# Kernel optimization log

Hardware: AMD Instinct MI355X
Metric: run time of the kernel (lower is better)

The kernel has to match this reference:

```python
import jax, jax.numpy as jnp
import numpy as np
import math

D_MODEL = 512
N_HEADS = 2
B, S = 2, 1024
THRESHOLD = 0.5  # kwargs default 'sparsity_threshold'


def setup_inputs() -> dict:
    key = jax.random.key(0)
    ks = jax.random.split(key, 10)
    D, H = D_MODEL, D_MODEL // 4
    std = 0.02
    return {
        "x": jax.random.normal(ks[0], (B, S, D), jnp.float32),
        "Wq": jax.random.normal(ks[1], (D, D), jnp.float32) * std,
        "Wk": jax.random.normal(ks[2], (D, D), jnp.float32) * std,
        "Wv": jax.random.normal(ks[3], (D, D), jnp.float32) * std,
        "Wo": jax.random.normal(ks[4], (D, D), jnp.float32) * std,
        "bo": jnp.zeros((D,), jnp.float32),
        "W1": jax.random.normal(ks[5], (D, H), jnp.float32) * std,
        "b1": jnp.zeros((H,), jnp.float32),
        "W2": jax.random.normal(ks[6], (H, 1), jnp.float32) * std,
        "b2": jnp.zeros((1,), jnp.float32),
    }


def reference(x, Wq, Wk, Wv, Wo, bo, W1, b1, W2, b2):
    Bsz, Seq, D = x.shape
    Hn = N_HEADS
    dh = D // Hn

    def split_heads(t):
        return t.reshape(Bsz, Seq, Hn, dh).transpose(0, 2, 1, 3)  # [B,H,S,dh]

    q = split_heads(x @ Wq)
    k = split_heads(x @ Wk)
    v = split_heads(x @ Wv)

    scores = jnp.einsum("bhid,bhjd->bhij", q, k) / math.sqrt(dh)  # [B,H,S,S]

    # head-mean features for the pairwise sparsity predictor (n_heads==2 => 2*dh == D)
    q_mean = q.mean(axis=1)  # [B,S,dh]
    k_mean = k.mean(axis=1)  # [B,S,dh]
    # Linear1 of cat([q_mean_i, k_mean_j]) splits into two halves of W1
    a = q_mean @ W1[:dh]   # [B,S,Dh4]
    c = k_mean @ W1[dh:]   # [B,S,Dh4]
    hidden = jax.nn.relu(a[:, :, None, :] + c[:, None, :, :] + b1)  # [B,S,S,Dh4]
    connection_probs = jax.nn.sigmoid(jnp.squeeze(hidden @ W2, -1) + b2[0])  # [B,S,S]

    mask = connection_probs > THRESHOLD  # [B,S,S]
    scores = jnp.where(mask[:, None, :, :], scores, jnp.float32(-1e9))
    attn = jax.nn.softmax(scores, axis=-1)  # dropout inactive in eval

    out = jnp.einsum("bhij,bhjd->bhid", attn, v)  # [B,H,S,dh]
    out = out.transpose(0, 2, 1, 3).reshape(Bsz, Seq, D)
    out = out @ Wo + bo
    return out
```

## Files before the change

### kernel.cpp

```cpp
#include <hip/hip_runtime.h>


typedef unsigned short u16t;
typedef __bf16 bf16x8 __attribute__((ext_vector_type(8)));
typedef float f32x4 __attribute__((ext_vector_type(4)));

#define B_SZ 2
#define S_SZ 1024
#define D_SZ 512
#define DH 256
#define HH 128

static __device__ __forceinline__ u16t f2b(float f) {
    unsigned int u = __builtin_bit_cast(unsigned int, f);
    u += 0x7FFFu + ((u >> 16) & 1u);
    return (u16t)(u >> 16);
}

static __device__ __forceinline__ f32x4 mfma16(bf16x8 a, bf16x8 b, f32x4 c) {
    return __builtin_amdgcn_mfma_f32_16x16x32_bf16(a, b, c, 0, 0, 0);
}

static __device__ __forceinline__ void gload16(const void* g, void* l) {
    __builtin_amdgcn_global_load_lds(
        (const __attribute__((address_space(1))) void*)g,
        (__attribute__((address_space(3))) void*)l, 16, 0, 0);
}

__global__ __launch_bounds__(256) void k_prep(
    const float* __restrict__ x,
    const float* __restrict__ Wq, const float* __restrict__ Wk,
    const float* __restrict__ Wv, const float* __restrict__ Wo,
    const float* __restrict__ W1,
    u16t* __restrict__ xb, u16t* __restrict__ WT, float* __restrict__ Beff)
{
    __shared__ float smf[1088];
    int bidx = blockIdx.x;
    int t = threadIdx.x;
    if (bidx < 1024) {
        int idx = (bidx * 256 + t) * 4;
        float4 v = *(const float4*)(x + idx);
        u16t* o = xb + idx;
        o[0] = f2b(v.x); o[1] = f2b(v.y); o[2] = f2b(v.z); o[3] = f2b(v.w);
    } else if (bidx < 2048) {
        int t2 = bidx - 1024;
        int z = t2 >> 8, rem = t2 & 255;
        int n0 = (rem & 15) * 32, k0 = (rem >> 4) * 32;
        const float* W = z == 0 ? Wq : z == 1 ? Wk : z == 2 ? Wv : Wo;
        u16t* WTz = WT + (size_t)z * D_SZ * D_SZ;
        float (*tile)[33] = (float(*)[33])smf;
        int r = t >> 3, c4 = (t & 7) * 4;
        float4 v = *(const float4*)(W + (size_t)(k0 + r) * D_SZ + n0 + c4);
        tile[r][c4] = v.x; tile[r][c4 + 1] = v.y; tile[r][c4 + 2] = v.z; tile[r][c4 + 3] = v.w;
        __syncthreads();
        u16t o[4];
        o[0] = f2b(tile[c4][r]); o[1] = f2b(tile[c4 + 1][r]);
        o[2] = f2b(tile[c4 + 2][r]); o[3] = f2b(tile[c4 + 3][r]);
        *(ushort4*)(WTz + (size_t)(n0 + r) * D_SZ + k0 + c4) = *(ushort4*)o;
    } else {
        int k = bidx - 2048;
        float* wm0 = smf;
        float* wm1 = smf + 256;
        const float* wrq = Wq + (size_t)k * D_SZ;
        const float* wrk = Wk + (size_t)k * D_SZ;
        wm0[t & 255] = 0.5f * (wrq[t & 255] + wrq[(t & 255) + DH]);
        wm1[t & 255] = 0.5f * (wrk[t & 255] + wrk[(t & 255) + DH]);
        __syncthreads();
        int half = t >> 7, hcol = t & 127;
        const float* wm = half ? wm1 : wm0;
        const float* W1h = W1 + (half ? (size_t)DH * HH : 0);
        float s = 0.f;
        for (int d = 0; d < 256; ++d) s += wm[d] * W1h[(size_t)d * HH + hcol];
        Beff[(size_t)k * 256 + half * 128 + hcol] = s;
    }
}

template<int MF, int NF>
static __device__ __forceinline__ void gemm_db(
    const u16t* __restrict__ A, int lda, const u16t* __restrict__ B, int ldb,
    int K, int tid, u16t* Als, u16t* Bls, f32x4 acc[MF][NF])
{
    const int w = tid >> 6, lane = tid & 63;
    const int lr = lane & 15, kg = lane >> 4;
    const int srow = lane >> 3, scol = (lane & 7) * 8;
    const int ABUF = MF * 4096;
    const int BBUF = NF * 1024;
    auto stage = [&](int bb, int k0) {
#pragma unroll
        for (int q = 0; q < MF * 2; ++q) {
            int ci = w * (MF * 2) + q;
            gload16(A + (size_t)(ci * 8 + srow) * lda + k0 + scol,
                    Als + bb * ABUF + ci * 512);
        }
#pragma unroll
        for (int q = 0; q < NF / 2; ++q) {
            int cj = w * (NF / 2) + q;
            gload16(B + (size_t)(cj * 8 + srow) * ldb + k0 + scol,
                    Bls + bb * BBUF + cj * 512);
        }
    };
    stage(0, 0);
    __syncthreads();
    const int nt = K / 64;
    for (int t = 0; t < nt; ++t) {
        int cur = t & 1;
        if (t + 1 < nt) stage(cur ^ 1, (t + 1) * 64);
        const u16t* Ab = Als + cur * ABUF;
        const u16t* Bb = Bls + cur * BBUF;
#pragma unroll
        for (int kk = 0; kk < 2; ++kk) {
            bf16x8 af[MF], bfr[NF];
#pragma unroll
            for (int fi = 0; fi < MF; ++fi)
                af[fi] = *(const bf16x8*)(&Ab[(w * (MF * 16) + fi * 16 + lr) * 64 + kk * 32 + kg * 8]);
#pragma unroll
            for (int fj = 0; fj < NF; ++fj)
                bfr[fj] = *(const bf16x8*)(&Bb[(fj * 16 + lr) * 64 + kk * 32 + kg * 8]);
#pragma unroll
            for (int fi = 0; fi < MF; ++fi)
#pragma unroll
                for (int fj = 0; fj < NF; ++fj)
                    acc[fi][fj] = mfma16(af[fi], bfr[fj], acc[fi][fj]);
        }
        __syncthreads();
    }
}


__global__ __launch_bounds__(256) void k_qkvac(
    const u16t* __restrict__ xb, const u16t* __restrict__ WT,
    const float* __restrict__ x, const float* __restrict__ Beff,
    const float* __restrict__ b1,
    u16t* __restrict__ qb, u16t* __restrict__ kb, u16t* __restrict__ vT,
    float* __restrict__ a, float* __restrict__ cc)
{
    __shared__ __align__(16) char sm[49152];
    int bid = blockIdx.x;
    int t = threadIdx.x;
    if (bid < 384) {
        u16t* Als = (u16t*)sm;
        u16t* Bls = (u16t*)(sm + 32768);
        int z = bid / 128, rem = bid & 127;
        int m0 = (rem >> 3) * 128, n0 = (rem & 7) * 64;
        const u16t* A = xb + (size_t)m0 * D_SZ;
        const u16t* Bt = WT + (size_t)z * D_SZ * D_SZ + (size_t)n0 * D_SZ;
        f32x4 acc[2][4] = {};
        gemm_db<2, 4>(A, D_SZ, Bt, D_SZ, D_SZ, t, Als, Bls, acc);
        int w = t >> 6, lane = t & 63, lr = lane & 15, kg = lane >> 4;
        if (z < 2) {
            u16t (*vls)[68] = (u16t(*)[68])sm;
            float scale = z == 0 ? 0.0625f : 1.0f;
#pragma unroll
            for (int fi = 0; fi < 2; ++fi)
#pragma unroll
                for (int fj = 0; fj < 4; ++fj)
#pragma unroll
                    for (int rr = 0; rr < 4; ++rr)
                        vls[w * 32 + fi * 16 + kg * 4 + rr][fj * 16 + lr]
                            = f2b(acc[fi][fj][rr] * scale);
            __syncthreads();
            u16t* dst = z == 0 ? qb : kb;
            int c8 = (t & 7) * 8, r0 = t >> 3;
#pragma unroll
            for (int p = 0; p < 4; ++p) {
                int r = r0 + p * 32;
                *(uint4*)(dst + (size_t)(m0 + r) * D_SZ + n0 + c8) = *(const uint4*)(&vls[r][c8]);
            }
        } else {
            u16t (*vls)[136] = (u16t(*)[136])sm;
#pragma unroll
            for (int fi = 0; fi < 2; ++fi)
#pragma unroll
                for (int fj = 0; fj < 4; ++fj)
#pragma unroll
                    for (int rr = 0; rr < 4; ++rr)
                        vls[fj * 16 + lr][w * 32 + fi * 16 + kg * 4 + rr] = f2b(acc[fi][fj][rr]);
            __syncthreads();
            int b = m0 >> 10, s0 = m0 & 1023;
            int cr = t >> 2, seg = t & 3;
            const u16t* srcp = &vls[cr][seg * 32];
            u16t* dstp = vT + (((size_t)(b * D_SZ + n0 + cr)) << 10) + s0 + seg * 32;
#pragma unroll
            for (int qq = 0; qq < 4; ++qq)
                *(uint4*)(dstp + qq * 8) = *(const uint4*)(srcp + qq * 8);
        }
    } else {
        float (*xs)[68] = (float(*)[68])sm;
        float (*bsT)[68] = (float(*)[68])(sm + 17408);
        int t2 = bid - 384;
        int r0 = (t2 & 31) * 64, n0 = (t2 >> 5) * 32;
        int ti = t >> 4, tj = t & 15;
        float acc[4][2] = {};
        for (int k0 = 0; k0 < 512; k0 += 64) {
            if (k0) __syncthreads();
#pragma unroll
            for (int p = 0; p < 4; ++p) {
                int idx = t + p * 256;
                int r = idx >> 4, c4 = (idx & 15) * 4;
                *(float4*)&xs[r][c4] = *(const float4*)(x + (size_t)(r0 + r) * D_SZ + k0 + c4);
            }
#pragma unroll
            for (int p = 0; p < 2; ++p) {
                int idx = t + p * 256;
                int k = idx >> 3, n4 = (idx & 7) * 4;
                float4 v = *(const float4*)(Beff + (size_t)(k0 + k) * 256 + n0 + n4);
                bsT[n4][k] = v.x; bsT[n4 + 1][k] = v.y; bsT[n4 + 2][k] = v.z; bsT[n4 + 3][k] = v.w;
            }
            __syncthreads();
#pragma unroll
            for (int kk = 0; kk < 16; ++kk) {
                float4 xv[4], bv[2];
#pragma unroll
                for (int ri = 0; ri < 4; ++ri) xv[ri] = *(const float4*)&xs[ti + 16 * ri][kk * 4];
#pragma unroll
                for (int rj = 0; rj < 2; ++rj) bv[rj] = *(const float4*)&bsT[tj + 16 * rj][kk * 4];
#pragma unroll
                for (int ri = 0; ri < 4; ++ri)
#pragma unroll
                    for (int rj = 0; rj < 2; ++rj)
                        acc[ri][rj] += xv[ri].x * bv[rj].x + xv[ri].y * bv[rj].y
                                     + xv[ri].z * bv[rj].z + xv[ri].w * bv[rj].w;
            }
        }
        bool isA = n0 < 128;
#pragma unroll
        for (int rj = 0; rj < 2; ++rj) {
            int col = n0 + tj + 16 * rj;
            float badd = isA ? b1[col] : 0.f;
#pragma unroll
            for (int ri = 0; ri < 4; ++ri) {
                int row = r0 + ti + 16 * ri;
                if (isA) a[(size_t)row * HH + col] = acc[ri][rj] + badd;
                else     cc[(size_t)row * HH + (col - 128)] = acc[ri][rj];
            }
        }
    }
}

__global__ __launch_bounds__(256) void k_mask(
    const float* __restrict__ a, const float* __restrict__ c,
    const float* __restrict__ W2, const float* __restrict__ b2,
    unsigned char* __restrict__ maskb)
{
    __shared__ __align__(16) float at[64][132];
    __shared__ __align__(16) float ct[64][132];
    __shared__ __align__(16) float w2s[128];
    int b = blockIdx.z, i0 = blockIdx.y * 64, j0 = blockIdx.x * 64;
    int t = threadIdx.x;
    if (t < 128) w2s[t] = W2[t];
#pragma unroll
    for (int p = 0; p < 8; ++p) {
        int idx = t + p * 256;
        int r = idx >> 5, c4 = (idx & 31) * 4;
        *(float4*)&at[r][c4] = *(const float4*)(a + ((size_t)(b * S_SZ + i0 + r)) * HH + c4);
        *(float4*)&ct[r][c4] = *(const float4*)(c + ((size_t)(b * S_SZ + j0 + r)) * HH + c4);
    }
    __syncthreads();
    float fb2 = b2[0];
    int ti = t >> 4, tj = t & 15;
    float acc[4][4];
#pragma unroll
    for (int ri = 0; ri < 4; ++ri)
#pragma unroll
        for (int rj = 0; rj < 4; ++rj) acc[ri][rj] = fb2;
#pragma unroll 2
    for (int h4 = 0; h4 < 32; ++h4) {
        float4 av[4], cv[4];
        float4 wv = ((const float4*)w2s)[h4];
#pragma unroll
        for (int ri = 0; ri < 4; ++ri) av[ri] = *(const float4*)&at[ti + 16 * ri][h4 * 4];
#pragma unroll
        for (int rj = 0; rj < 4; ++rj) cv[rj] = *(const float4*)&ct[tj + 16 * rj][h4 * 4];
#pragma unroll
        for (int ri = 0; ri < 4; ++ri)
#pragma unroll
            for (int rj = 0; rj < 4; ++rj) {
                acc[ri][rj] += fmaxf(av[ri].x + cv[rj].x, 0.f) * wv.x;
                acc[ri][rj] += fmaxf(av[ri].y + cv[rj].y, 0.f) * wv.y;
                acc[ri][rj] += fmaxf(av[ri].z + cv[rj].z, 0.f) * wv.z;
                acc[ri][rj] += fmaxf(av[ri].w + cv[rj].w, 0.f) * wv.w;
            }
    }
#pragma unroll
    for (int ri = 0; ri < 4; ++ri)
#pragma unroll
        for (int rj = 0; rj < 4; ++rj) {
            int i = i0 + ti + 16 * ri, j = j0 + tj + 16 * rj;
            maskb[((size_t)b << 20) + ((size_t)i << 10) + j] = acc[ri][rj] > 0.f ? 1 : 0;
        }
}

__global__ __launch_bounds__(256) void k_scores(
    const u16t* __restrict__ qb, const u16t* __restrict__ kb,
    const unsigned char* __restrict__ maskb, u16t* __restrict__ P,
    float* __restrict__ lpart)
{
    __shared__ __align__(16) u16t sm[16384];
    u16t* Als = sm;
    u16t* Bls = sm + 8192;
    int bh = blockIdx.z, b = bh >> 1, h = bh & 1;
    int jb = blockIdx.x;
    int m0 = blockIdx.y * 64, n0 = jb * 64;
    const u16t* A = qb + (size_t)b * S_SZ * D_SZ + (size_t)m0 * D_SZ + h * DH;
    const u16t* Bt = kb + (size_t)b * S_SZ * D_SZ + (size_t)n0 * D_SZ + h * DH;
    f32x4 acc[1][4] = {};
    gemm_db<1, 4>(A, D_SZ, Bt, D_SZ, DH, threadIdx.x, Als, Bls, acc);
    int w = threadIdx.x >> 6, lane = threadIdx.x & 63, lr = lane & 15, kg = lane >> 4;
#pragma unroll
    for (int rr = 0; rr < 4; ++rr) {
        int i = m0 + w * 16 + kg * 4 + rr;
        float rs = 0.f;
#pragma unroll
        for (int fj = 0; fj < 4; ++fj) {
            int j = n0 + fj * 16 + lr;
            bool msk = maskb[((size_t)b << 20) + ((size_t)i << 10) + j] != 0;
            float e = msk ? __expf(acc[0][fj][rr]) : 0.f;
            acc[0][fj][rr] = e;
            rs += e;
        }
        rs += __shfl_xor(rs, 1); rs += __shfl_xor(rs, 2);
        rs += __shfl_xor(rs, 4); rs += __shfl_xor(rs, 8);
        if (lr == 0) lpart[((size_t)(jb * 4 + bh) << 10) + i] = rs;
    }
    __syncthreads();
    u16t (*vls)[68] = (u16t(*)[68])sm;
#pragma unroll
    for (int fj = 0; fj < 4; ++fj)
#pragma unroll
        for (int rr = 0; rr < 4; ++rr)
            vls[w * 16 + kg * 4 + rr][fj * 16 + lr] = f2b(acc[0][fj][rr]);
    __syncthreads();
    int r = threadIdx.x >> 2, c16 = (threadIdx.x & 3) * 16;
    u16t* dstp = P + ((size_t)bh << 20) + ((size_t)(m0 + r) << 10) + n0 + c16;
    *(uint4*)dstp = *(const uint4*)(&vls[r][c16]);
    *(uint4*)(dstp + 8) = *(const uint4*)(&vls[r][c16 + 8]);
}

__global__ __launch_bounds__(256) void k_pv(
    const u16t* __restrict__ P, const u16t* __restrict__ vT,
    const float* __restrict__ lpart, u16t* __restrict__ ao)
{
    __shared__ __align__(16) u16t sm[12288];
    __shared__ float invl[64];
    u16t* Als = sm;
    u16t* Bls = sm + 8192;
    int bh = blockIdx.z, b = bh >> 1, h = bh & 1;
    int m0 = blockIdx.y * 64, n0 = blockIdx.x * 32;
    int t = threadIdx.x;
    if (t < 64) {
        float l = 0.f;
        for (int jb = 0; jb < 16; ++jb)
            l += lpart[((size_t)(jb * 4 + bh) << 10) + m0 + t];
        invl[t] = l > 0.f ? 1.0f / l : 0.f;
    }
    const u16t* A = P + ((size_t)bh << 20) + (size_t)m0 * S_SZ;
    const u16t* Bt = vT + ((size_t)(b * D_SZ + h * DH + n0)) * S_SZ;
    f32x4 acc[1][2] = {};
    gemm_db<1, 2>(A, S_SZ, Bt, S_SZ, S_SZ, t, Als, Bls, acc);
    int w = t >> 6, lane = t & 63, lr = lane & 15, kg = lane >> 4;
    u16t (*ols)[40] = (u16t(*)[40])sm;
#pragma unroll
    for (int fj = 0; fj < 2; ++fj)
#pragma unroll
        for (int rr = 0; rr < 4; ++rr) {
            int rl = w * 16 + kg * 4 + rr;
            ols[rl][fj * 16 + lr] = f2b(acc[0][fj][rr] * invl[rl]);
        }
    __syncthreads();
    int r = t >> 2, c8 = (t & 3) * 8;
    *(uint4*)(ao + ((size_t)(b * S_SZ + m0 + r)) * D_SZ + h * DH + n0 + c8)
        = *(const uint4*)(&ols[r][c8]);
}

__global__ __launch_bounds__(256) void k_out(
    const u16t* __restrict__ ao, const u16t* __restrict__ WoT,
    const float* __restrict__ bo, float* __restrict__ out)
{
    __shared__ __align__(16) u16t sm[12288];
    u16t* Als = sm;
    u16t* Bls = sm + 8192;
    int m0 = blockIdx.y * 64, n0 = blockIdx.x * 32;
    const u16t* A = ao + (size_t)m0 * D_SZ;
    const u16t* Bt = WoT + (size_t)n0 * D_SZ;
    f32x4 acc[1][2] = {};
    gemm_db<1, 2>(A, D_SZ, Bt, D_SZ, D_SZ, threadIdx.x, Als, Bls, acc);
    int w = threadIdx.x >> 6, lane = threadIdx.x & 63, lr = lane & 15, kg = lane >> 4;
    float (*ols)[36] = (float(*)[36])sm;
#pragma unroll
    for (int fj = 0; fj < 2; ++fj)
#pragma unroll
        for (int rr = 0; rr < 4; ++rr) {
            int rl = w * 16 + kg * 4 + rr;
            ols[rl][fj * 16 + lr] = acc[0][fj][rr] + bo[n0 + fj * 16 + lr];
        }
    __syncthreads();
    int r0 = threadIdx.x >> 3, c4 = (threadIdx.x & 7) * 4;
#pragma unroll
    for (int p = 0; p < 2; ++p) {
        int r = r0 + p * 32;
        *(float4*)(out + (size_t)(m0 + r) * D_SZ + n0 + c4) = *(const float4*)(&ols[r][c4]);
    }
}

extern "C" void kernel_launch(void* const* d_in, const int* in_sizes, int n_in,
                              void* d_out, int out_size, void* d_ws, size_t ws_size,
                              hipStream_t stream)
{
    const float* x  = (const float*)d_in[0];
    const float* Wq = (const float*)d_in[1];
    const float* Wk = (const float*)d_in[2];
    const float* Wv = (const float*)d_in[3];
    const float* Wo = (const float*)d_in[4];
    const float* bo = (const float*)d_in[5];
    const float* W1 = (const float*)d_in[6];
    const float* b1 = (const float*)d_in[7];
    const float* W2 = (const float*)d_in[8];
    const float* b2 = (const float*)d_in[9];
    float* out = (float*)d_out;

    char* ws = (char*)d_ws;
    size_t off = 0;
    auto carve = [&](size_t bytes) { void* p = ws + off; off += (bytes + 255) & ~(size_t)255; return p; };
    u16t* xb   = (u16t*)carve((size_t)2048 * 512 * 2);
    u16t* WT   = (u16t*)carve((size_t)4 * 512 * 512 * 2);
    u16t* qb   = (u16t*)carve((size_t)2048 * 512 * 2);
    u16t* kb   = (u16t*)carve((size_t)2048 * 512 * 2);
    u16t* vT   = (u16t*)carve((size_t)2 * 512 * 1024 * 2);
    float* Beff = (float*)carve((size_t)512 * 256 * 4);
    float* a   = (float*)carve((size_t)2048 * 128 * 4);
    float* c   = (float*)carve((size_t)2048 * 128 * 4);
    unsigned char* maskb = (unsigned char*)carve((size_t)2 * 1024 * 1024);
    u16t* P    = (u16t*)carve((size_t)4 * 1024 * 1024 * 2);
    float* lpart = (float*)carve((size_t)16 * 4 * 1024 * 4);
    u16t* ao   = (u16t*)carve((size_t)2048 * 512 * 2);
    (void)ws_size;

    k_prep<<<dim3(2560), dim3(256), 0, stream>>>(x, Wq, Wk, Wv, Wo, W1, xb, WT, Beff);
    k_qkvac<<<dim3(640), dim3(256), 0, stream>>>(xb, WT, x, Beff, b1, qb, kb, vT, a, c);
    k_mask<<<dim3(16, 16, 2), dim3(256), 0, stream>>>(a, c, W2, b2, maskb);
    k_scores<<<dim3(16, 16, 4), dim3(256), 0, stream>>>(qb, kb, maskb, P, lpart);
    k_pv<<<dim3(8, 16, 4), dim3(256), 0, stream>>>(P, vT, lpart, ao);
    k_out<<<dim3(16, 32), dim3(256), 0, stream>>>(ao, WT + (size_t)3 * 512 * 512, bo, out);
}
```

Baseline: 104.8 us.

## Fuse mask predictor into scores kernel and compute both heads per block

The separate mask kernel is merged into the scores kernel. Each block first computes its 64x64 mask tile in shared memory, then runs the QK^T GEMM for both heads over the full 512-wide row, writing exp-scores and partial row sums for each head. This removes one launch and the global mask byte array write/read, and the mask is computed once for both heads. The cost is fewer blocks (512 instead of 1024), larger shared memory use (about 54KB), and more sequential work per block, which may lower occupancy.

After: 103.2 us. No clear change (-1.6%).

```diff
diff --git a/kernel.cpp b/kernel.cpp
--- a/kernel.cpp
+++ b/kernel.cpp
@@ -237,103 +237,143 @@
     }
 }
 
-__global__ __launch_bounds__(256) void k_mask(
+__global__ __launch_bounds__(256) void k_scores(
+    const u16t* __restrict__ qb, const u16t* __restrict__ kb,
     const float* __restrict__ a, const float* __restrict__ c,
     const float* __restrict__ W2, const float* __restrict__ b2,
-    unsigned char* __restrict__ maskb)
-{
-    __shared__ __align__(16) float at[64][132];
-    __shared__ __align__(16) float ct[64][132];
-    __shared__ __align__(16) float w2s[128];
-    int b = blockIdx.z, i0 = blockIdx.y * 64, j0 = blockIdx.x * 64;
+    u16t* __restrict__ P, float* __restrict__ lpart)
+{
+    __shared__ __align__(16) char sm[55296];
+    float (*at)[132] = (float(*)[132])sm;
+    float (*ct)[132] = (float(*)[132])(sm + 33792);
+    unsigned char (*msk)[64] = (unsigned char(*)[64])(sm + 50688);
+    float* w2s = (float*)(sm + 54784);
+    int b = blockIdx.z, mt = blockIdx.y, jb = blockIdx.x;
+    int m0 = mt * 64, j0 = jb * 64;
     int t = threadIdx.x;
     if (t < 128) w2s[t] = W2[t];
 #pragma unroll
     for (int p = 0; p < 8; ++p) {
         int idx = t + p * 256;
         int r = idx >> 5, c4 = (idx & 31) * 4;
-        *(float4*)&at[r][c4] = *(const float4*)(a + ((size_t)(b * S_SZ + i0 + r)) * HH + c4);
-        *(float4*)&ct[r][c4] = *(const float4*)(c + ((size_t)(b * S_SZ + j0 + r)) * HH + c4);
-    }
-    __syncthreads();
+        *(float4*)&at[r][c4] = *(const float4*)(a + ((size_t)(b * S_SZ + m0 + r)) * HH + c4);
+    }
     float fb2 = b2[0];
     int ti = t >> 4, tj = t & 15;
-    float acc[4][4];
-#pragma unroll
-    for (int ri = 0; ri < 4; ++ri)
-#pragma unroll
-        for (int rj = 0; rj < 4; ++rj) acc[ri][rj] = fb2;
+#pragma unroll
+    for (int jh = 0; jh < 2; ++jh) {
+        __syncthreads();
+#pragma unroll
+        for (int p = 0; p < 4; ++p) {
+            int idx = t + p * 256;
+            int r = idx >> 5, c4 = (idx & 31) * 4;
+            *(float4*)&ct[r][c4] =
+                *(const float4*)(c + ((size_t)(b * S_SZ + j0 + jh * 32 + r)) * HH + c4);
+        }
+        __syncthreads();
+        float accm[4][2];
+#pragma unroll
+        for (int ri = 0; ri < 4; ++ri)
+#pragma unroll
+            for (int rj = 0; rj < 2; ++rj) accm[ri][rj] = fb2;
 #pragma unroll 2
-    for (int h4 = 0; h4 < 32; ++h4) {
-        float4 av[4], cv[4];
-        float4 wv = ((const float4*)w2s)[h4];
-#pragma unroll
-        for (int ri = 0; ri < 4; ++ri) av[ri] = *(const float4*)&at[ti + 16 * ri][h4 * 4];
-#pragma unroll
-        for (int rj = 0; rj < 4; ++rj) cv[rj] = *(const float4*)&ct[tj + 16 * rj][h4 * 4];
+        for (int h4 = 0; h4 < 32; ++h4) {
+            float4 wv = ((const float4*)w2s)[h4];
+            float4 av[4], cv[2];
+#pragma unroll
+            for (int ri = 0; ri < 4; ++ri) av[ri] = *(const float4*)&at[ti + 16 * ri][h4 * 4];
+#pragma unroll
+            for (int rj = 0; rj < 2; ++rj) cv[rj] = *(const float4*)&ct[tj + 16 * rj][h4 * 4];
+#pragma unroll
+            for (int ri = 0; ri < 4; ++ri)
+#pragma unroll
+                for (int rj = 0; rj < 2; ++rj) {
+                    accm[ri][rj] += fmaxf(av[ri].x + cv[rj].x, 0.f) * wv.x;
+                    accm[ri][rj] += fmaxf(av[ri].y + cv[rj].y, 0.f) * wv.y;
+                    accm[ri][rj] += fmaxf(av[ri].z + cv[rj].z, 0.f) * wv.z;
+                    accm[ri][rj] += fmaxf(av[ri].w + cv[rj].w, 0.f) * wv.w;
+                }
+        }
 #pragma unroll
         for (int ri = 0; ri < 4; ++ri)
 #pragma unroll
-            for (int rj = 0; rj < 4; ++rj) {
-                acc[ri][rj] += fmaxf(av[ri].x + cv[rj].x, 0.f) * wv.x;
-                acc[ri][rj] += fmaxf(av[ri].y + cv[rj].y, 0.f) * wv.y;
-                acc[ri][rj] += fmaxf(av[ri].z + cv[rj].z, 0.f) * wv.z;
-                acc[ri][rj] += fmaxf(av[ri].w + cv[rj].w, 0.f) * wv.w;
-            }
-    }
-#pragma unroll
-    for (int ri = 0; ri < 4; ++ri)
-#pragma unroll
-        for (int rj = 0; rj < 4; ++rj) {
-            int i = i0 + ti + 16 * ri, j = j0 + tj + 16 * rj;
-            maskb[((size_t)b << 20) + ((size_t)i << 10) + j] = acc[ri][rj] > 0.f ? 1 : 0;
-        }
-}
-
-__global__ __launch_bounds__(256) void k_scores(
-    const u16t* __restrict__ qb, const u16t* __restrict__ kb,
-    const unsigned char* __restrict__ maskb, u16t* __restrict__ P,
-    float* __restrict__ lpart)
-{
-    __shared__ __align__(16) u16t sm[16384];
-    u16t* Als = sm;
-    u16t* Bls = sm + 8192;
-    int bh = blockIdx.z, b = bh >> 1, h = bh & 1;
-    int jb = blockIdx.x;
-    int m0 = blockIdx.y * 64, n0 = jb * 64;
-    const u16t* A = qb + (size_t)b * S_SZ * D_SZ + (size_t)m0 * D_SZ + h * DH;
-    const u16t* Bt = kb + (size_t)b * S_SZ * D_SZ + (size_t)n0 * D_SZ + h * DH;
-    f32x4 acc[1][4] = {};
-    gemm_db<1, 4>(A, D_SZ, Bt, D_SZ, DH, threadIdx.x, Als, Bls, acc);
-    int w = threadIdx.x >> 6, lane = threadIdx.x & 63, lr = lane & 15, kg = lane >> 4;
-#pragma unroll
-    for (int rr = 0; rr < 4; ++rr) {
-        int i = m0 + w * 16 + kg * 4 + rr;
-        float rs = 0.f;
-#pragma unroll
-        for (int fj = 0; fj < 4; ++fj) {
-            int j = n0 + fj * 16 + lr;
-            bool msk = maskb[((size_t)b << 20) + ((size_t)i << 10) + j] != 0;
-            float e = msk ? __expf(acc[0][fj][rr]) : 0.f;
-            acc[0][fj][rr] = e;
-            rs += e;
-        }
-        rs += __shfl_xor(rs, 1); rs += __shfl_xor(rs, 2);
-        rs += __shfl_xor(rs, 4); rs += __shfl_xor(rs, 8);
-        if (lr == 0) lpart[((size_t)(jb * 4 + bh) << 10) + i] = rs;
+            for (int rj = 0; rj < 2; ++rj)
+                msk[ti + 16 * ri][jh * 32 + tj + 16 * rj] = accm[ri][rj] > 0.f ? 1 : 0;
     }
     __syncthreads();
+    u16t* Als = (u16t*)sm;
+    u16t* Bls = (u16t*)(sm + 16384);
+    const u16t* A = qb + (size_t)(b * S_SZ + m0) * D_SZ;
+    const u16t* B = kb + (size_t)(b * S_SZ + j0) * D_SZ;
+    const int w = t >> 6, lane = t & 63, lr = lane & 15, kg = lane >> 4;
+    const int srow = lane >> 3, scol = (lane & 7) * 8;
+    auto stage = [&](int bb, int k0) {
+#pragma unroll
+        for (int q = 0; q < 2; ++q) {
+            int ci = w * 2 + q;
+            gload16(A + (size_t)(ci * 8 + srow) * D_SZ + k0 + scol, Als + bb * 4096 + ci * 512);
+            gload16(B + (size_t)(ci * 8 + srow) * D_SZ + k0 + scol, Bls + bb * 4096 + ci * 512);
+        }
+    };
+    f32x4 acc0[4] = {}, acc1[4] = {};
+    stage(0, 0);
+    __syncthreads();
+#pragma unroll
+    for (int t8 = 0; t8 < 8; ++t8) {
+        int cur = t8 & 1;
+        if (t8 < 7) stage(cur ^ 1, (t8 + 1) * 64);
+        const u16t* Ab = Als + cur * 4096;
+        const u16t* Bb = Bls + cur * 4096;
+#pragma unroll
+        for (int kk = 0; kk < 2; ++kk) {
+            bf16x8 af = *(const bf16x8*)(&Ab[(w * 16 + lr) * 64 + kk * 32 + kg * 8]);
+            bf16x8 bfr[4];
+#pragma unroll
+            for (int fj = 0; fj < 4; ++fj)
+                bfr[fj] = *(const bf16x8*)(&Bb[(fj * 16 + lr) * 64 + kk * 32 + kg * 8]);
+            if (t8 < 4) {
+#pragma unroll
+                for (int fj = 0; fj < 4; ++fj) acc0[fj] = mfma16(af, bfr[fj], acc0[fj]);
+            } else {
+#pragma unroll
+                for (int fj = 0; fj < 4; ++fj) acc1[fj] = mfma16(af, bfr[fj], acc1[fj]);
+            }
+        }
+        __syncthreads();
+    }
     u16t (*vls)[68] = (u16t(*)[68])sm;
 #pragma unroll
-    for (int fj = 0; fj < 4; ++fj)
-#pragma unroll
-        for (int rr = 0; rr < 4; ++rr)
-            vls[w * 16 + kg * 4 + rr][fj * 16 + lr] = f2b(acc[0][fj][rr]);
-    __syncthreads();
-    int r = threadIdx.x >> 2, c16 = (threadIdx.x & 3) * 16;
-    u16t* dstp = P + ((size_t)bh << 20) + ((size_t)(m0 + r) << 10) + n0 + c16;
-    *(uint4*)dstp = *(const uint4*)(&vls[r][c16]);
-    *(uint4*)(dstp + 8) = *(const uint4*)(&vls[r][c16 + 8]);
+    for (int h = 0; h < 2; ++h) {
+#pragma unroll
+        for (int rr = 0; rr < 4; ++rr) {
+            int il = w * 16 + kg * 4 + rr;
+            float rs = 0.f;
+#pragma unroll
+            for (int fj = 0; fj < 4; ++fj) {
+                int jl = fj * 16 + lr;
+                float s = h ? acc1[fj][rr] : acc0[fj][rr];
+                float e = msk[il][jl] ? __expf(s) : 0.f;
+                if (h) acc1[fj][rr] = e; else acc0[fj][rr] = e;
+                rs += e;
+            }
+            rs += __shfl_xor(rs, 1); rs += __shfl_xor(rs, 2);
+            rs += __shfl_xor(rs, 4); rs += __shfl_xor(rs, 8);
+            if (lr == 0)
+                lpart[((size_t)(jb * 4 + b * 2 + h) << 10) + m0 + il] = rs;
+        }
+#pragma unroll
+        for (int fj = 0; fj < 4; ++fj)
+#pragma unroll
+            for (int rr = 0; rr < 4; ++rr)
+                vls[w * 16 + kg * 4 + rr][fj * 16 + lr]
+                    = f2b(h ? acc1[fj][rr] : acc0[fj][rr]);
+        __syncthreads();
+        int r = t >> 2, c16 = (t & 3) * 16;
+        u16t* dstp = P + ((size_t)(b * 2 + h) << 20) + ((size_t)(m0 + r) << 10) + j0 + c16;
+        *(uint4*)dstp = *(const uint4*)(&vls[r][c16]);
+        *(uint4*)(dstp + 8) = *(const uint4*)(&vls[r][c16 + 8]);
+        __syncthreads();
+    }
 }
 
 __global__ __launch_bounds__(256) void k_pv(
@@ -429,7 +469,6 @@
     float* Beff = (float*)carve((size_t)512 * 256 * 4);
     float* a   = (float*)carve((size_t)2048 * 128 * 4);
     float* c   = (float*)carve((size_t)2048 * 128 * 4);
-    unsigned char* maskb = (unsigned char*)carve((size_t)2 * 1024 * 1024);
     u16t* P    = (u16t*)carve((size_t)4 * 1024 * 1024 * 2);
     float* lpart = (float*)carve((size_t)16 * 4 * 1024 * 4);
     u16t* ao   = (u16t*)carve((size_t)2048 * 512 * 2);
@@ -437,8 +476,7 @@
 
     k_prep<<<dim3(2560), dim3(256), 0, stream>>>(x, Wq, Wk, Wv, Wo, W1, xb, WT, Beff);
     k_qkvac<<<dim3(640), dim3(256), 0, stream>>>(xb, WT, x, Beff, b1, qb, kb, vT, a, c);
-    k_mask<<<dim3(16, 16, 2), dim3(256), 0, stream>>>(a, c, W2, b2, maskb);
-    k_scores<<<dim3(16, 16, 4), dim3(256), 0, stream>>>(qb, kb, maskb, P, lpart);
+    k_scores<<<dim3(16, 16, 2), dim3(256), 0, stream>>>(qb, kb, a, c, W2, b2, P, lpart);
     k_pv<<<dim3(8, 16, 4), dim3(256), 0, stream>>>(P, vT, lpart, ao);
     k_out<<<dim3(16, 32), dim3(256), 0, stream>>>(ao, WT + (size_t)3 * 512 * 512, bo, out);
 }
```
